# Optimization experiments

Hardware: AMD Instinct MI355X
Metric: run time of the kernel (lower is better)

The kernel has to match this reference:

```python
import jax, jax.numpy as jnp
import numpy as np

B, S, HIDDEN = 2, 2048, 2048
NUM_HEADS = 16
HEAD_DIM = 128
ROPE_BASE = 10000.0


def _rope_cos_sin(positions):
    # positions: [B, S] int -> cos/sin [B, 1, S, HEAD_DIM]
    inv_freq = 1.0 / (ROPE_BASE ** (jnp.arange(0, HEAD_DIM, 2, dtype=jnp.float32) / HEAD_DIM))
    freqs = positions.astype(jnp.float32)[..., None] * inv_freq  # [B, S, D/2]
    emb = jnp.concatenate([freqs, freqs], axis=-1)  # [B, S, D]
    return jnp.cos(emb)[:, None, :, :], jnp.sin(emb)[:, None, :, :]


def _rotate_half(x, cos, sin):
    half = x.shape[-1] // 2
    x1, x2 = x[..., :half], x[..., half:]
    return jnp.concatenate([-x2, x1], axis=-1) * sin + x * cos


def setup_inputs() -> dict:
    key = jax.random.key(0)
    ks = jax.random.split(key, 6)
    hidden_states = jax.random.normal(ks[0], (B, S, HIDDEN), dtype=jnp.float32)
    positions = jnp.arange(B * S, dtype=jnp.int64 if jax.config.x64_enabled else jnp.int32).reshape(B, S)
    scale = 0.02
    Wq = jax.random.normal(ks[1], (HIDDEN, NUM_HEADS * HEAD_DIM), dtype=jnp.float32) * scale
    Wk = jax.random.normal(ks[2], (HIDDEN, NUM_HEADS * HEAD_DIM), dtype=jnp.float32) * scale
    Wv = jax.random.normal(ks[3], (HIDDEN, NUM_HEADS * HEAD_DIM), dtype=jnp.float32) * scale
    Wo = jax.random.normal(ks[4], (NUM_HEADS * HEAD_DIM, HIDDEN), dtype=jnp.float32) * scale
    bq = jnp.zeros((NUM_HEADS * HEAD_DIM,), dtype=jnp.float32)
    bk = jnp.zeros((NUM_HEADS * HEAD_DIM,), dtype=jnp.float32)
    bv = jnp.zeros((NUM_HEADS * HEAD_DIM,), dtype=jnp.float32)
    return {"positions": positions, "hidden_states": hidden_states,
            "Wq": Wq, "bq": bq, "Wk": Wk, "bk": bk, "Wv": Wv, "bv": bv, "Wo": Wo}


def reference(positions, hidden_states, Wq, bq, Wk, bk, Wv, bv, Wo):
    b, s, _ = hidden_states.shape
    # projections
    q = hidden_states @ Wq + bq  # [B, S, H*D]
    k = hidden_states @ Wk + bk
    v = hidden_states @ Wv + bv
    # -> [B, H, S, D]
    q = q.reshape(b, s, NUM_HEADS, HEAD_DIM).transpose(0, 2, 1, 3)
    k = k.reshape(b, s, NUM_HEADS, HEAD_DIM).transpose(0, 2, 1, 3)
    v = v.reshape(b, s, NUM_HEADS, HEAD_DIM).transpose(0, 2, 1, 3)
    # RoPE
    cos, sin = _rope_cos_sin(positions)
    q = _rotate_half(q, cos, sin)
    k = _rotate_half(k, cos, sin)
    # scaled dot-product attention (no mask)
    scaling = HEAD_DIM ** -0.5
    scores = jnp.einsum('bhqd,bhkd->bhqk', q, k) * scaling
    attn = jax.nn.softmax(scores, axis=-1)
    out = jnp.einsum('bhqk,bhkd->bhqd', attn, v)
    out = out.transpose(0, 2, 1, 3).reshape(b, s, NUM_HEADS * HEAD_DIM)
    return out @ Wo
```

## Files before the change

kernel.cpp:

```cpp
#include <hip/hip_runtime.h>
#include <cstdint>
#include <cstddef>

typedef unsigned short u16;
typedef __attribute__((ext_vector_type(8))) unsigned short u16x8;
typedef __attribute__((ext_vector_type(8))) short bf16x8;
typedef __attribute__((ext_vector_type(4))) float f32x4;

#define MFMA_BF16(a, b, c) __builtin_amdgcn_mfma_f32_16x16x32_bf16((a), (b), (c), 0, 0, 0)

__device__ __forceinline__ u16 f2bf(float f) {
  union { float f; uint32_t u; } v; v.f = f;
  uint32_t r = v.u + 0x7fffu + ((v.u >> 16) & 1u);
  return (u16)(r >> 16);
}
__device__ __forceinline__ float bf2f(u16 u) {
  union { uint32_t u; float f; } v; v.u = ((uint32_t)u) << 16;
  return v.f;
}
__device__ __forceinline__ void gl2lds16(const void* g, void* l) {
  __builtin_amdgcn_global_load_lds((__attribute__((address_space(1))) const void*)g,
                                   (__attribute__((address_space(3))) void*)l, 16, 0, 0);
}


__global__ __launch_bounds__(256) void cvt_kernel(const float* __restrict__ in,
                                                  u16* __restrict__ out) {
  int idx = blockIdx.x * 256 + threadIdx.x;
  float4 a = ((const float4*)in)[(size_t)idx * 2];
  float4 b = ((const float4*)in)[(size_t)idx * 2 + 1];
  u16x8 o;
  o[0] = f2bf(a.x); o[1] = f2bf(a.y); o[2] = f2bf(a.z); o[3] = f2bf(a.w);
  o[4] = f2bf(b.x); o[5] = f2bf(b.y); o[6] = f2bf(b.z); o[7] = f2bf(b.w);
  *(u16x8*)(out + (size_t)idx * 8) = o;
}

__global__ __launch_bounds__(256) void trans_kernel(const float* __restrict__ in,
                                                    u16* __restrict__ out) {
  __shared__ float tile[64][65];
  int t = threadIdx.x;
  int r0 = blockIdx.y * 64, c0 = blockIdx.x * 64;
#pragma unroll
  for (int i = 0; i < 16; ++i) {
    int idx = i * 256 + t; int r = idx >> 6, c = idx & 63;
    tile[r][c] = in[(size_t)(r0 + r) * 2048 + c0 + c];
  }
  __syncthreads();
#pragma unroll
  for (int i = 0; i < 16; ++i) {
    int idx = i * 256 + t; int r = idx >> 6, c = idx & 63;
    out[(size_t)(c0 + r) * 2048 + r0 + c] = f2bf(tile[c][r]);
  }
}

__global__ __launch_bounds__(256) void rope_table_kernel(const int* __restrict__ pos,
                                                         float* __restrict__ cosT,
                                                         float* __restrict__ sinT) {
  int idx = blockIdx.x * 256 + threadIdx.x;
  int i = idx & 63, t = idx >> 6;
  double ang = (double)pos[t] * exp(-(double)i * (9.210340371976184 / 64.0));
  double s, c;
  sincos(ang, &s, &c);
  cosT[idx] = (float)c;
  sinT[idx] = (float)s;
}

__global__ __launch_bounds__(256) void rope_kernel(u16* __restrict__ Q,
                                                   u16* __restrict__ Kk,
                                                   const float* __restrict__ cosT,
                                                   const float* __restrict__ sinT) {
  int idx = blockIdx.x * 256 + threadIdx.x;
  int d = idx & 63, h = (idx >> 6) & 15, tok = idx >> 10;
  int b = tok >> 11, s = tok & 2047;
  size_t base = ((size_t)((b * 16 + h) * 2048 + s)) * 128;
  float c = cosT[(tok << 6) + d], sn = sinT[(tok << 6) + d];
  const float sc = 0.08838834764831845f;
  float q1 = bf2f(Q[base + d]), q2 = bf2f(Q[base + d + 64]);
  Q[base + d]      = f2bf((q1 * c - q2 * sn) * sc);
  Q[base + d + 64] = f2bf((q2 * c + q1 * sn) * sc);
  float k1 = bf2f(Kk[base + d]), k2 = bf2f(Kk[base + d + 64]);
  Kk[base + d]      = f2bf(k1 * c - k2 * sn);
  Kk[base + d + 64] = f2bf(k2 * c + k1 * sn);
}

__global__ __launch_bounds__(256) void vtrans_kernel(const u16* __restrict__ V,
                                                     u16* __restrict__ Vt) {
  __shared__ u16 tile[128][72];
  int t = threadIdx.x;
  int bh = blockIdx.x >> 5, st = blockIdx.x & 31;
  const u16* src = V + ((size_t)bh * 2048 + st * 64) * 128;
#pragma unroll
  for (int i = 0; i < 4; ++i) {
    int idx = i * 256 + t;
    int s = idx >> 4;
    int d0 = (idx & 15) << 3;
    u16x8 v = *(const u16x8*)(src + (size_t)s * 128 + d0);
#pragma unroll
    for (int j = 0; j < 8; ++j) tile[d0 + j][s] = v[j];
  }
  __syncthreads();
  u16* dst = Vt + (size_t)bh * 128 * 2048 + st * 64;
#pragma unroll
  for (int i = 0; i < 4; ++i) {
    int idx = i * 256 + t;
    int d = idx >> 3;
    int s0 = (idx & 7) << 3;
    u16x8 o;
#pragma unroll
    for (int j = 0; j < 8; ++j) o[j] = tile[d][s0 + j];
    *(u16x8*)(dst + (size_t)d * 2048 + s0) = o;
  }
}


__global__ __launch_bounds__(256) void gemm1_kernel(
    const u16* __restrict__ A,
    const u16* __restrict__ Bt,
    const float* __restrict__ bq, const float* __restrict__ bk, const float* __restrict__ bv,
    u16* __restrict__ Qo, u16* __restrict__ Ko, u16* __restrict__ Vo) {
  __shared__ u16 sA[128 * 32], sB[128 * 32];
  const int K = 2048;
  int t = threadIdx.x, lane = t & 63, wid = t >> 6;
  int bm = blockIdx.x & 31, bn = blockIdx.x >> 5;
  int m0 = bm << 7, n0 = bn << 7;
  int wr = wid >> 1, wc = wid & 1;
  int fr = lane & 15, fq = lane >> 4;

  const f32x4 vzero = {0.f, 0.f, 0.f, 0.f};
  f32x4 acc[4][4];
#pragma unroll
  for (int m = 0; m < 4; ++m)
#pragma unroll
    for (int n = 0; n < 4; ++n) acc[m][n] = vzero;

  int arow = t >> 2, acol = (t & 3) << 3;
  const u16* ga0 = A + (size_t)(m0 + arow) * K + acol;
  const u16* ga1 = ga0 + (size_t)64 * K;
  const u16* gb0 = Bt + (size_t)(n0 + arow) * K + acol;
  const u16* gb1 = gb0 + (size_t)64 * K;
  u16* lA0 = sA + t * 8; u16* lA1 = sA + 2048 + t * 8;
  u16* lB0 = sB + t * 8; u16* lB1 = sB + 2048 + t * 8;

  for (int k0 = 0; k0 < K; k0 += 32) {
    gl2lds16(ga0 + k0, lA0);
    gl2lds16(ga1 + k0, lA1);
    gl2lds16(gb0 + k0, lB0);
    gl2lds16(gb1 + k0, lB1);
    __syncthreads();
    bf16x8 af[4], bfv[4];
#pragma unroll
    for (int m = 0; m < 4; ++m)
      af[m] = *(const bf16x8*)(sA + ((wr * 64 + m * 16 + fr) * 32 + fq * 8));
#pragma unroll
    for (int n = 0; n < 4; ++n)
      bfv[n] = *(const bf16x8*)(sB + ((wc * 64 + n * 16 + fr) * 32 + fq * 8));
#pragma unroll
    for (int m = 0; m < 4; ++m)
#pragma unroll
      for (int n = 0; n < 4; ++n)
        acc[m][n] = MFMA_BF16(af[m], bfv[n], acc[m][n]);
    __syncthreads();
  }
#pragma unroll
  for (int n = 0; n < 4; ++n) {
    int col = n0 + wc * 64 + n * 16 + fr;
    int which = col >> 11;
    int cin = col & 2047;
    const float* bp = (which == 0) ? bq : (which == 1) ? bk : bv;
    u16* dst = (which == 0) ? Qo : (which == 1) ? Ko : Vo;
    float bias = bp[cin];
    int h = cin >> 7, d = cin & 127;
#pragma unroll
    for (int m = 0; m < 4; ++m) {
      int row = m0 + wr * 64 + m * 16 + fq * 4;
#pragma unroll
      for (int r = 0; r < 4; ++r) {
        int tok = row + r;
        int b = tok >> 11, s = tok & 2047;
        dst[((size_t)((b * 16 + h) * 2048 + s) << 7) + d] = f2bf(acc[m][n][r] + bias);
      }
    }
  }
}

__global__ __launch_bounds__(256) void gemm2_kernel(
    const u16* __restrict__ A,
    const u16* __restrict__ Bt,
    float* __restrict__ C) {
  __shared__ u16 sA[128 * 32], sB[128 * 32];
  const int K = 2048;
  int t = threadIdx.x, lane = t & 63, wid = t >> 6;
  int bm = blockIdx.x & 31, bn = blockIdx.x >> 5;
  int m0 = bm << 7, n0 = bn << 7;
  int wr = wid >> 1, wc = wid & 1;
  int fr = lane & 15, fq = lane >> 4;

  const f32x4 vzero = {0.f, 0.f, 0.f, 0.f};
  f32x4 acc[4][4];
#pragma unroll
  for (int m = 0; m < 4; ++m)
#pragma unroll
    for (int n = 0; n < 4; ++n) acc[m][n] = vzero;

  int arow = t >> 2, acol = (t & 3) << 3;
  const u16* ga0 = A + (size_t)(m0 + arow) * K + acol;
  const u16* ga1 = ga0 + (size_t)64 * K;
  const u16* gb0 = Bt + (size_t)(n0 + arow) * K + acol;
  const u16* gb1 = gb0 + (size_t)64 * K;
  u16* lA0 = sA + t * 8; u16* lA1 = sA + 2048 + t * 8;
  u16* lB0 = sB + t * 8; u16* lB1 = sB + 2048 + t * 8;

  for (int k0 = 0; k0 < K; k0 += 32) {
    gl2lds16(ga0 + k0, lA0);
    gl2lds16(ga1 + k0, lA1);
    gl2lds16(gb0 + k0, lB0);
    gl2lds16(gb1 + k0, lB1);
    __syncthreads();
    bf16x8 af[4], bfv[4];
#pragma unroll
    for (int m = 0; m < 4; ++m)
      af[m] = *(const bf16x8*)(sA + ((wr * 64 + m * 16 + fr) * 32 + fq * 8));
#pragma unroll
    for (int n = 0; n < 4; ++n)
      bfv[n] = *(const bf16x8*)(sB + ((wc * 64 + n * 16 + fr) * 32 + fq * 8));
#pragma unroll
    for (int m = 0; m < 4; ++m)
#pragma unroll
      for (int n = 0; n < 4; ++n)
        acc[m][n] = MFMA_BF16(af[m], bfv[n], acc[m][n]);
    __syncthreads();
  }
#pragma unroll
  for (int n = 0; n < 4; ++n) {
    int col = n0 + wc * 64 + n * 16 + fr;
#pragma unroll
    for (int m = 0; m < 4; ++m) {
      int row = m0 + wr * 64 + m * 16 + fq * 4;
#pragma unroll
      for (int r = 0; r < 4; ++r)
        C[(size_t)(row + r) * 2048 + col] = acc[m][n][r];
    }
  }
}

__global__ __launch_bounds__(512) void attn_kernel(
    const u16* __restrict__ Q_,
    const u16* __restrict__ K_,
    const u16* __restrict__ Vt_,
    u16* __restrict__ AO) {
  __shared__ u16 sK[2][64 * 128];
  __shared__ u16 sV[2][128 * 64];
  __shared__ u16 sP[8][32 * 64];
  int t = threadIdx.x, lane = t & 63, wid = t >> 6;
  int fr = lane & 15, fq = lane >> 4;
  int qt = blockIdx.x & 7, bh = blockIdx.x >> 3;
  int q0 = qt << 8;
  const u16* Qb = Q_ + (size_t)bh * 2048 * 128;
  const char* Kc = (const char*)(K_ + (size_t)bh * 2048 * 128);
  const char* Vc = (const char*)(Vt_ + (size_t)bh * 128 * 2048);

  bf16x8 qf[2][4];
#pragma unroll
  for (int m = 0; m < 2; ++m) {
    const u16* qp = Qb + (size_t)(q0 + wid * 32 + m * 16 + fr) * 128 + fq * 8;
#pragma unroll
    for (int kk = 0; kk < 4; ++kk) qf[m][kk] = *(const bf16x8*)(qp + kk * 32);
  }

  int kgoff[2], kldst[2], vgoff[2], vldst[2];
#pragma unroll
  for (int i = 0; i < 2; ++i) {
    int kr = i * 32 + (t >> 4);
    kgoff[i] = kr * 256 + (((t & 15) << 4) ^ ((kr & 7) << 4));
    kldst[i] = i * 8192 + t * 16;
    int vr = i * 64 + (t >> 3);
    vgoff[i] = vr * 4096 + (((t & 7) << 4) ^ ((vr & 7) << 4));
    vldst[i] = i * 8192 + t * 16;
  }

#define STAGE(tt, bb)                                                          \
  {                                                                            \
    size_t ko = (size_t)(tt) * 16384;                                          \
    size_t vo = (size_t)(tt) * 128;                                            \
    _Pragma("unroll")                                                          \
    for (int i = 0; i < 2; ++i)                                                \
      gl2lds16(Kc + ko + kgoff[i], (char*)sK[bb] + kldst[i]);                  \
    _Pragma("unroll")                                                          \
    for (int i = 0; i < 2; ++i)                                                \
      gl2lds16(Vc + vo + vgoff[i], (char*)sV[bb] + vldst[i]);                  \
  }

  float mrun[2][4], lrun[2][4];
#pragma unroll
  for (int m = 0; m < 2; ++m)
#pragma unroll
    for (int r = 0; r < 4; ++r) { mrun[m][r] = -1e30f; lrun[m][r] = 0.f; }
  const f32x4 vzero = {0.f, 0.f, 0.f, 0.f};
  f32x4 oacc[2][8];
#pragma unroll
  for (int m = 0; m < 2; ++m)
#pragma unroll
    for (int fd = 0; fd < 8; ++fd) oacc[m][fd] = vzero;

  char* sPw = (char*)sP[wid];

  STAGE(0, 0);
  __syncthreads();

  for (int tile = 0; tile < 32; ++tile) {
    int cur = tile & 1;
    if (tile < 31) STAGE(tile + 1, cur ^ 1);
    const char* Kb_ = (const char*)sK[cur];
    const char* Vb_ = (const char*)sV[cur];

    f32x4 sacc[2][4];
#pragma unroll
    for (int m = 0; m < 2; ++m)
#pragma unroll
      for (int n = 0; n < 4; ++n) sacc[m][n] = vzero;
    __builtin_amdgcn_s_setprio(1);
#pragma unroll
    for (int n = 0; n < 4; ++n) {
      int krow = n * 16 + fr;
      int swz = (krow & 7) << 4;
      const char* kbase = Kb_ + krow * 256;
#pragma unroll
      for (int kk = 0; kk < 4; ++kk) {
        bf16x8 kf = *(const bf16x8*)(kbase + ((kk * 64 + fq * 16) ^ swz));
        sacc[0][n] = MFMA_BF16(qf[0][kk], kf, sacc[0][n]);
        sacc[1][n] = MFMA_BF16(qf[1][kk], kf, sacc[1][n]);
      }
    }
    __builtin_amdgcn_s_setprio(0);

    float pmax[2][4];
#pragma unroll
    for (int m = 0; m < 2; ++m)
#pragma unroll
      for (int r = 0; r < 4; ++r) {
        float v = fmaxf(fmaxf(sacc[m][0][r], sacc[m][1][r]),
                        fmaxf(sacc[m][2][r], sacc[m][3][r]));
        v = fmaxf(v, __shfl_xor(v, 1));
        v = fmaxf(v, __shfl_xor(v, 2));
        v = fmaxf(v, __shfl_xor(v, 4));
        v = fmaxf(v, __shfl_xor(v, 8));
        pmax[m][r] = v;
      }
    int ok = 1;
#pragma unroll
    for (int m = 0; m < 2; ++m)
#pragma unroll
      for (int r = 0; r < 4; ++r)
        ok &= (pmax[m][r] <= mrun[m][r] + 8.f) ? 1 : 0;
    if (!__all(ok)) {
#pragma unroll
      for (int m = 0; m < 2; ++m)
#pragma unroll
        for (int r = 0; r < 4; ++r) {
          float mn = fmaxf(mrun[m][r], pmax[m][r]);
          float scl = __expf(mrun[m][r] - mn);
          mrun[m][r] = mn;
          lrun[m][r] *= scl;
#pragma unroll
          for (int fd = 0; fd < 8; ++fd) oacc[m][fd][r] *= scl;
        }
    }
    float rs[2][4] = {{0.f, 0.f, 0.f, 0.f}, {0.f, 0.f, 0.f, 0.f}};
#pragma unroll
    for (int m = 0; m < 2; ++m)
#pragma unroll
      for (int n = 0; n < 4; ++n)
#pragma unroll
        for (int r = 0; r < 4; ++r) {
          float p = __expf(sacc[m][n][r] - mrun[m][r]);
          rs[m][r] += p;
          int q = m * 16 + fq * 4 + r;
          *(u16*)(sPw + q * 128 + ((((n * 16 + fr) << 1)) ^ ((q & 7) << 4))) = f2bf(p);
        }
#pragma unroll
    for (int m = 0; m < 2; ++m)
#pragma unroll
      for (int r = 0; r < 4; ++r) {
        float s = rs[m][r];
        s += __shfl_xor(s, 1);
        s += __shfl_xor(s, 2);
        s += __shfl_xor(s, 4);
        s += __shfl_xor(s, 8);
        lrun[m][r] += s;
      }

    bf16x8 pf[2][2];
#pragma unroll
    for (int m = 0; m < 2; ++m)
#pragma unroll
      for (int kk = 0; kk < 2; ++kk)
        pf[m][kk] = *(const bf16x8*)(sPw + (m * 16 + fr) * 128 +
                                     ((kk * 64 + fq * 16) ^ ((fr & 7) << 4)));
    __builtin_amdgcn_s_setprio(1);
#pragma unroll
    for (int fd = 0; fd < 8; ++fd) {
      int vrow = fd * 16 + fr;
      int vswz = (vrow & 7) << 4;
      const char* vbase = Vb_ + vrow * 128;
#pragma unroll
      for (int kk = 0; kk < 2; ++kk) {
        bf16x8 vf = *(const bf16x8*)(vbase + ((kk * 64 + fq * 16) ^ vswz));
        oacc[0][fd] = MFMA_BF16(pf[0][kk], vf, oacc[0][fd]);
        oacc[1][fd] = MFMA_BF16(pf[1][kk], vf, oacc[1][fd]);
      }
    }
    __builtin_amdgcn_s_setprio(0);
    __syncthreads();
  }
#undef STAGE

  int h = bh & 15, b = bh >> 4;
#pragma unroll
  for (int m = 0; m < 2; ++m)
#pragma unroll
    for (int r = 0; r < 4; ++r) {
      float inv = 1.f / lrun[m][r];
      int tok = b * 2048 + q0 + wid * 32 + m * 16 + fq * 4 + r;
#pragma unroll
      for (int fd = 0; fd < 8; ++fd) {
        int col = h * 128 + fd * 16 + fr;
        AO[(size_t)tok * 2048 + col] = f2bf(oacc[m][fd][r] * inv);
      }
    }
}


extern "C" void kernel_launch(void* const* d_in, const int* in_sizes, int n_in,
                              void* d_out, int out_size, void* d_ws, size_t ws_size,
                              hipStream_t stream) {
  (void)in_sizes; (void)n_in; (void)out_size; (void)ws_size;
  const int*   positions = (const int*)d_in[0];
  const float* hidden    = (const float*)d_in[1];
  const float* Wq = (const float*)d_in[2];
  const float* bq = (const float*)d_in[3];
  const float* Wk = (const float*)d_in[4];
  const float* bk = (const float*)d_in[5];
  const float* Wv = (const float*)d_in[6];
  const float* bv = (const float*)d_in[7];
  const float* Wo = (const float*)d_in[8];
  float* out = (float*)d_out;

  char* ws = (char*)d_ws;
  u16*   Xb   = (u16*)(ws);
  u16*   Wt   = (u16*)(ws + 16777216);
  u16*   Wot  = (u16*)(ws + 41943040);
  u16*   Qb   = (u16*)(ws + 50331648);
  u16*   Kb   = (u16*)(ws + 67108864);
  u16*   Vb   = (u16*)(ws + 83886080);
  u16*   Vtb  = (u16*)(ws + 100663296);
  u16*   AO   = (u16*)(ws + 117440512);
  float* cosT = (float*)(ws + 134217728);
  float* sinT = (float*)(ws + 135266304);

  cvt_kernel<<<4096, 256, 0, stream>>>(hidden, Xb);
  trans_kernel<<<dim3(32, 32), 256, 0, stream>>>(Wq, Wt);
  trans_kernel<<<dim3(32, 32), 256, 0, stream>>>(Wk, Wt + (size_t)2048 * 2048);
  trans_kernel<<<dim3(32, 32), 256, 0, stream>>>(Wv, Wt + (size_t)2 * 2048 * 2048);
  trans_kernel<<<dim3(32, 32), 256, 0, stream>>>(Wo, Wot);
  rope_table_kernel<<<1024, 256, 0, stream>>>(positions, cosT, sinT);
  gemm1_kernel<<<1536, 256, 0, stream>>>(Xb, Wt, bq, bk, bv, Qb, Kb, Vb);
  rope_kernel<<<16384, 256, 0, stream>>>(Qb, Kb, cosT, sinT);
  vtrans_kernel<<<1024, 256, 0, stream>>>(Vb, Vtb);
  attn_kernel<<<256, 512, 0, stream>>>(Qb, Kb, Vtb, AO);
  gemm2_kernel<<<512, 256, 0, stream>>>(AO, Wot, out);
}
```

Baseline: 473.7 us.

## Rewrite QKV GEMM with 256x256 tiles, double-buffered swizzled LDS and interleaved prefetch

The fused QKV projection GEMM moves from 128x128 tiles with 256 threads to 256x256 tiles with 512 threads and a K-step of 64. Global-to-LDS loads for the next K tile are double-buffered and interleaved with the MFMA phases, using explicit vmcnt/lgkmcnt waits, raw barriers and setprio. LDS rows are XOR-swizzled to avoid bank conflicts. This aims to hide load latency and raise data reuse, at the cost of more LDS and registers per block and fewer blocks (384) across the CUs.

Measured after the change: 520.3 us. 1.1x slower.

```diff
diff --git a/kernel.cpp b/kernel.cpp
--- a/kernel.cpp
+++ b/kernel.cpp
@@ -113,75 +113,160 @@
 }
 
 
-__global__ __launch_bounds__(256) void gemm1_kernel(
+#define G1_STAGE_A(kt, kh)                                                     \
+  { _Pragma("unroll") for (int j = 0; j < 2; ++j)                              \
+      gl2lds16(gAsrc[j] + (size_t)(kt) * 64 + (kh) * 32,                       \
+               sA[(kt) & 1][kh] + ldso[j]); }
+#define G1_STAGE_B(kt, kh)                                                     \
+  { _Pragma("unroll") for (int j = 0; j < 2; ++j)                              \
+      gl2lds16(gBsrc[j] + (size_t)(kt) * 64 + (kh) * 32,                       \
+               sB[(kt) & 1][kh] + ldso[j]); }
+#define G1_BAR()  __builtin_amdgcn_s_barrier()
+#define G1_WL0()  do { asm volatile("s_waitcnt lgkmcnt(0)" ::: "memory");      \
+                       __builtin_amdgcn_sched_barrier(0); } while (0)
+#define G1_WV(n)  asm volatile("s_waitcnt vmcnt(" #n ")" ::: "memory")
+
+__global__ __launch_bounds__(512, 2) void gemm1_kernel(
     const u16* __restrict__ A,
     const u16* __restrict__ Bt,
     const float* __restrict__ bq, const float* __restrict__ bk, const float* __restrict__ bv,
     u16* __restrict__ Qo, u16* __restrict__ Ko, u16* __restrict__ Vo) {
-  __shared__ u16 sA[128 * 32], sB[128 * 32];
+  __shared__ char sA[2][2][16384];
+  __shared__ char sB[2][2][16384];
   const int K = 2048;
   int t = threadIdx.x, lane = t & 63, wid = t >> 6;
-  int bm = blockIdx.x & 31, bn = blockIdx.x >> 5;
-  int m0 = bm << 7, n0 = bn << 7;
-  int wr = wid >> 1, wc = wid & 1;
   int fr = lane & 15, fq = lane >> 4;
-
-  const f32x4 vzero = {0.f, 0.f, 0.f, 0.f};
-  f32x4 acc[4][4];
-#pragma unroll
-  for (int m = 0; m < 4; ++m)
-#pragma unroll
-    for (int n = 0; n < 4; ++n) acc[m][n] = vzero;
-
-  int arow = t >> 2, acol = (t & 3) << 3;
-  const u16* ga0 = A + (size_t)(m0 + arow) * K + acol;
-  const u16* ga1 = ga0 + (size_t)64 * K;
-  const u16* gb0 = Bt + (size_t)(n0 + arow) * K + acol;
-  const u16* gb1 = gb0 + (size_t)64 * K;
-  u16* lA0 = sA + t * 8; u16* lA1 = sA + 2048 + t * 8;
-  u16* lB0 = sB + t * 8; u16* lB1 = sB + 2048 + t * 8;
-
-  for (int k0 = 0; k0 < K; k0 += 32) {
-    gl2lds16(ga0 + k0, lA0);
-    gl2lds16(ga1 + k0, lA1);
-    gl2lds16(gb0 + k0, lB0);
-    gl2lds16(gb1 + k0, lB1);
-    __syncthreads();
-    bf16x8 af[4], bfv[4];
-#pragma unroll
-    for (int m = 0; m < 4; ++m)
-      af[m] = *(const bf16x8*)(sA + ((wr * 64 + m * 16 + fr) * 32 + fq * 8));
-#pragma unroll
-    for (int n = 0; n < 4; ++n)
-      bfv[n] = *(const bf16x8*)(sB + ((wc * 64 + n * 16 + fr) * 32 + fq * 8));
-#pragma unroll
-    for (int m = 0; m < 4; ++m)
-#pragma unroll
-      for (int n = 0; n < 4; ++n)
-        acc[m][n] = MFMA_BF16(af[m], bfv[n], acc[m][n]);
-    __syncthreads();
-  }
+  int bm = blockIdx.x & 15, bn = blockIdx.x >> 4;
+  int m0 = bm << 8, n0 = bn << 8;
+  int wr = wid >> 2, wc = wid & 3;
+
+  float bias[4]; const float* bps[4]; u16* dsts[4]; int hh[4], dd[4];
 #pragma unroll
   for (int n = 0; n < 4; ++n) {
     int col = n0 + wc * 64 + n * 16 + fr;
     int which = col >> 11;
     int cin = col & 2047;
-    const float* bp = (which == 0) ? bq : (which == 1) ? bk : bv;
-    u16* dst = (which == 0) ? Qo : (which == 1) ? Ko : Vo;
-    float bias = bp[cin];
-    int h = cin >> 7, d = cin & 127;
-#pragma unroll
-    for (int m = 0; m < 4; ++m) {
-      int row = m0 + wr * 64 + m * 16 + fq * 4;
+    bps[n] = (which == 0) ? bq : (which == 1) ? bk : bv;
+    dsts[n] = (which == 0) ? Qo : (which == 1) ? Ko : Vo;
+    bias[n] = bps[n][cin];
+    hh[n] = cin >> 7; dd[n] = cin & 127;
+  }
+  G1_WV(0);
+
+  int ldso[2]; const u16* gAsrc[2]; const u16* gBsrc[2];
+#pragma unroll
+  for (int j = 0; j < 2; ++j) {
+    int o = wid * 2048 + j * 1024 + lane * 16;
+    int p = o >> 7;
+    int v = ((o >> 4) & 7) ^ (p & 7);
+    int row = 2 * p + (v >> 2);
+    int kofs = (v & 3) * 8;
+    ldso[j] = o;
+    gAsrc[j] = A + (size_t)(m0 + row) * K + kofs;
+    gBsrc[j] = Bt + (size_t)(n0 + row) * K + kofs;
+  }
+
+  int aoff[8], boff[4];
+#pragma unroll
+  for (int m = 0; m < 8; ++m) {
+    int r = wr * 128 + m * 16 + fr;
+    int p = r >> 1;
+    aoff[m] = p * 128 + ((((r & 1) << 6) | (fq << 4)) ^ ((p & 7) << 4));
+  }
+#pragma unroll
+  for (int n = 0; n < 4; ++n) {
+    int r = wc * 64 + n * 16 + fr;
+    int p = r >> 1;
+    boff[n] = p * 128 + ((((r & 1) << 6) | (fq << 4)) ^ ((p & 7) << 4));
+  }
+
+  const f32x4 vzero = {0.f, 0.f, 0.f, 0.f};
+  f32x4 acc[8][4];
+#pragma unroll
+  for (int m = 0; m < 8; ++m)
+#pragma unroll
+    for (int n = 0; n < 4; ++n) acc[m][n] = vzero;
+
+  G1_STAGE_A(0, 0); G1_STAGE_B(0, 0); G1_STAGE_A(0, 1); G1_STAGE_B(0, 1);
+  G1_WV(4);
+  G1_BAR();
+
+  for (int kt = 0; kt < 32; ++kt) {
+    int cur = kt & 1;
+    bf16x8 a[4], b[4], a2[4];
+#pragma unroll
+    for (int m = 0; m < 4; ++m) a[m] = *(const bf16x8*)(sA[cur][0] + aoff[m]);
+#pragma unroll
+    for (int n = 0; n < 4; ++n) b[n] = *(const bf16x8*)(sB[cur][0] + boff[n]);
+    if (kt < 31) G1_STAGE_A(kt + 1, 0);
+    G1_BAR();
+    G1_WL0();
+    __builtin_amdgcn_s_setprio(1);
+#pragma unroll
+    for (int m = 0; m < 4; ++m)
+#pragma unroll
+      for (int n = 0; n < 4; ++n) acc[m][n] = MFMA_BF16(a[m], b[n], acc[m][n]);
+    __builtin_amdgcn_s_setprio(0);
+    G1_BAR();
+#pragma unroll
+    for (int m = 0; m < 4; ++m) a2[m] = *(const bf16x8*)(sA[cur][0] + aoff[m + 4]);
+    if (kt < 31) { G1_STAGE_B(kt + 1, 0); G1_WV(4); }
+    else         { G1_WV(0); }
+    G1_BAR();
+    G1_WL0();
+    __builtin_amdgcn_s_setprio(1);
+#pragma unroll
+    for (int m = 0; m < 4; ++m)
+#pragma unroll
+      for (int n = 0; n < 4; ++n) acc[m + 4][n] = MFMA_BF16(a2[m], b[n], acc[m + 4][n]);
+    __builtin_amdgcn_s_setprio(0);
+    G1_BAR();
+#pragma unroll
+    for (int m = 0; m < 4; ++m) a[m] = *(const bf16x8*)(sA[cur][1] + aoff[m]);
+#pragma unroll
+    for (int n = 0; n < 4; ++n) b[n] = *(const bf16x8*)(sB[cur][1] + boff[n]);
+    if (kt < 31) G1_STAGE_A(kt + 1, 1);
+    G1_BAR();
+    G1_WL0();
+    __builtin_amdgcn_s_setprio(1);
+#pragma unroll
+    for (int m = 0; m < 4; ++m)
+#pragma unroll
+      for (int n = 0; n < 4; ++n) acc[m][n] = MFMA_BF16(a[m], b[n], acc[m][n]);
+    __builtin_amdgcn_s_setprio(0);
+    G1_BAR();
+#pragma unroll
+    for (int m = 0; m < 4; ++m) a2[m] = *(const bf16x8*)(sA[cur][1] + aoff[m + 4]);
+    if (kt < 31) { G1_STAGE_B(kt + 1, 1); G1_WV(4); }
+    G1_BAR();
+    G1_WL0();
+    __builtin_amdgcn_s_setprio(1);
+#pragma unroll
+    for (int m = 0; m < 4; ++m)
+#pragma unroll
+      for (int n = 0; n < 4; ++n) acc[m + 4][n] = MFMA_BF16(a2[m], b[n], acc[m + 4][n]);
+    __builtin_amdgcn_s_setprio(0);
+    G1_BAR();
+  }
+
+#pragma unroll
+  for (int n = 0; n < 4; ++n) {
+    u16* dst = dsts[n];
+    float bs = bias[n];
+    int h = hh[n], d = dd[n];
+#pragma unroll
+    for (int m = 0; m < 8; ++m) {
+      int row = m0 + wr * 128 + m * 16 + fq * 4;
 #pragma unroll
       for (int r = 0; r < 4; ++r) {
         int tok = row + r;
-        int b = tok >> 11, s = tok & 2047;
-        dst[((size_t)((b * 16 + h) * 2048 + s) << 7) + d] = f2bf(acc[m][n][r] + bias);
+        int b_ = tok >> 11, s = tok & 2047;
+        dst[((size_t)((b_ * 16 + h) * 2048 + s) << 7) + d] = f2bf(acc[m][n][r] + bs);
       }
     }
   }
 }
+
 
 __global__ __launch_bounds__(256) void gemm2_kernel(
     const u16* __restrict__ A,
@@ -463,7 +548,7 @@
   trans_kernel<<<dim3(32, 32), 256, 0, stream>>>(Wv, Wt + (size_t)2 * 2048 * 2048);
   trans_kernel<<<dim3(32, 32), 256, 0, stream>>>(Wo, Wot);
   rope_table_kernel<<<1024, 256, 0, stream>>>(positions, cosT, sinT);
-  gemm1_kernel<<<1536, 256, 0, stream>>>(Xb, Wt, bq, bk, bv, Qb, Kb, Vb);
+  gemm1_kernel<<<384, 512, 0, stream>>>(Xb, Wt, bq, bk, bv, Qb, Kb, Vb);
   rope_kernel<<<16384, 256, 0, stream>>>(Qb, Kb, cosT, sinT);
   vtrans_kernel<<<1024, 256, 0, stream>>>(Vb, Vtb);
   attn_kernel<<<256, 512, 0, stream>>>(Qb, Kb, Vtb, AO);
```
